# Kernel tuning notes

Measured on AMD Instinct MI355X. Metric: run time of the kernel, lower is better.

Reference implementation:

```python
import jax, jax.numpy as jnp
import numpy as np

NNZ = 131072      # number of sparse 2-tuples
M = 1048576       # number of precomputed product triples for spspmm
EMB = 128


def _mlp(x, W0, b0, W1, b1):
    # MLP(emb_dim, emb_dim, mlplayer=2, tailact=True): linear+ReLU twice
    h = jax.nn.relu(x @ W0 + b0)
    return jax.nn.relu(h @ W1 + b1)


def setup_inputs() -> dict:
    key = jax.random.key(0)
    ks = jax.random.split(key, 8)
    s = 1.0 / np.sqrt(EMB)
    Xv = jax.random.normal(ks[0], (NNZ, EMB), dtype=jnp.float32)
    W1_0 = jax.random.normal(ks[1], (EMB, EMB), dtype=jnp.float32) * s
    W1_1 = jax.random.normal(ks[2], (EMB, EMB), dtype=jnp.float32) * s
    W2_0 = jax.random.normal(ks[3], (EMB, EMB), dtype=jnp.float32) * s
    W2_1 = jax.random.normal(ks[4], (EMB, EMB), dtype=jnp.float32) * s
    b = jnp.zeros((EMB,), dtype=jnp.float32)
    ind_a = jax.random.randint(ks[5], (M,), 0, NNZ, dtype=jnp.int32)
    ind_b = jax.random.randint(ks[6], (M,), 0, NNZ, dtype=jnp.int32)
    ind_out = jax.random.randint(ks[7], (M,), 0, NNZ, dtype=jnp.int32)
    return {"Xv": Xv, "W1_0": W1_0, "b1_0": b, "W1_1": W1_1, "b1_1": b,
            "W2_0": W2_0, "b2_0": b, "W2_1": W2_1, "b2_1": b,
            "ind_a": ind_a, "ind_b": ind_b, "ind_out": ind_out}


def reference(Xv, W1_0, b1_0, W1_1, b1_1, W2_0, b2_0, W2_1, b2_1,
              ind_a, ind_b, ind_out):
    # tuplewise MLP transforms
    X1 = _mlp(Xv, W1_0, b1_0, W1_1, b1_1)   # [nnz, emb]
    X2 = _mlp(Xv, W2_0, b2_0, W2_1, b2_1)   # [nnz, emb]
    # messagepassing_tuple with sum aggregation (sparse spspmm via
    # precomputed product triples): out[t] += X1[a] * X2[b]
    prod = X1[ind_a] * X2[ind_b]            # [M, emb]
    out = jax.ops.segment_sum(prod, ind_out, num_segments=NNZ)  # [nnz, emb]
    return out
```

## Files before the change

kernel.cpp:

```cpp
#include <hip/hip_runtime.h>
#include <hip/hip_bf16.h>

#define NNZ 131072
#define MT  1048576
#define EMB 128
#define CAP 32

typedef __attribute__((ext_vector_type(8))) short  short8;
typedef __attribute__((ext_vector_type(4))) float  floatx4;

__device__ __forceinline__ ushort f2bf(float f) {
    unsigned u = __float_as_uint(f);
    u = (u + 0x7FFFu + ((u >> 16) & 1u)) >> 16;
    return (ushort)u;
}

__global__ __launch_bounds__(256) void pack_hist_kernel(
    const float* __restrict__ W10, const float* __restrict__ W11,
    const float* __restrict__ W20, const float* __restrict__ W21,
    ushort* __restrict__ Wpk,
    const int* __restrict__ io, int* __restrict__ cnt)
{
    if (blockIdx.x < 32) {
        int s = blockIdx.x * 256 + threadIdx.x;
        int L = s >> 11, sl = s & 2047;
        const float* W = (L == 0) ? W10 : (L == 1) ? W11 : (L == 2) ? W20 : W21;
        int lane = sl & 63, nk = sl >> 6;
        int col  = (nk >> 2) * 16 + (lane & 15);
        int krow = (nk & 3) * 32 + (lane >> 4) * 8;
        short8 w;
        #pragma unroll
        for (int j = 0; j < 8; ++j)
            w[j] = (short)f2bf(W[(krow + j) * EMB + col]);
        *(short8*)&Wpk[(size_t)s * 8] = w;
    } else {
        int i = (blockIdx.x - 32) * 256 + threadIdx.x;
        atomicAdd(&cnt[io[i]], 1);
    }
}

__global__ __launch_bounds__(512) void mlp_fused(
    const float* __restrict__ Xv, const ushort* __restrict__ Wpk,
    const float* __restrict__ b10, const float* __restrict__ b11,
    const float* __restrict__ b20, const float* __restrict__ b21,
    ushort* __restrict__ X1b, ushort* __restrict__ X2b,
    int do_scatter, const int* __restrict__ io, const int* __restrict__ ia,
    const int* __restrict__ ib, int* __restrict__ cur, int2* __restrict__ pairs)
{
    __shared__ ushort Wp[16384];
    __shared__ ushort Hs[16384];

    const int tid  = threadIdx.x;
    const int wave = tid >> 6;
    const int lane = tid & 63;
    const int g    = lane >> 4;
    const int r    = lane & 15;
    const int rowbase = blockIdx.x * 128 + wave * 16;
    char* hw = (char*)(Hs + wave * 2048);

    auto doScatter = [&]() {
        int base = (int)blockIdx.x * 1024 + tid;
        #pragma unroll
        for (int k = 0; k < 2; ++k) {
            int t = base + k * 512;
            int o = io[t];
            int p = atomicAdd(&cur[o], 1);
            pairs[(size_t)o * CAP + p] = make_int2(ia[t], ib[t]);
        }
    };
    const bool scatFirst = do_scatter && (blockIdx.x & 1);
    if (scatFirst) doScatter();

    short8 af[4];
    {
        const float* xsrc = Xv + (size_t)(rowbase + r) * EMB;
        #pragma unroll
        for (int kt = 0; kt < 4; ++kt) {
            const float4* p = (const float4*)(xsrc + kt * 32 + g * 8);
            float4 v0 = p[0], v1 = p[1];
            short8 a;
            a[0] = (short)f2bf(v0.x); a[1] = (short)f2bf(v0.y);
            a[2] = (short)f2bf(v0.z); a[3] = (short)f2bf(v0.w);
            a[4] = (short)f2bf(v1.x); a[5] = (short)f2bf(v1.y);
            a[6] = (short)f2bf(v1.z); a[7] = (short)f2bf(v1.w);
            af[kt] = a;
        }
    }

    auto stageW = [&](int L) {
        const ushort* src = Wpk + (size_t)L * 16384;
        #pragma unroll
        for (int s = tid; s < 2048; s += 512)
            *(short8*)&Wp[s * 8] = *(const short8*)&src[(size_t)s * 8];
    };

    floatx4 acc[8];
    auto runMFMA = [&](const short8* a4) {
        #pragma unroll
        for (int n = 0; n < 8; ++n) {
            floatx4 c = {0.f, 0.f, 0.f, 0.f};
            #pragma unroll
            for (int kt = 0; kt < 4; ++kt) {
                short8 b = *(const short8*)&Wp[((n * 4 + kt) * 64 + lane) * 8];
                c = __builtin_amdgcn_mfma_f32_16x16x32_bf16(b, a4[kt], c, 0, 0, 0);
            }
            acc[n] = c;
        }
    };

    auto epi = [&](const float* __restrict__ bias) {
        #pragma unroll
        for (int n = 0; n < 8; ++n) {
            float4 bv = *(const float4*)&bias[n * 16 + g * 4];
            ushort4 w;
            w.x = f2bf(fmaxf(acc[n][0] + bv.x, 0.f));
            w.y = f2bf(fmaxf(acc[n][1] + bv.y, 0.f));
            w.z = f2bf(fmaxf(acc[n][2] + bv.z, 0.f));
            w.w = f2bf(fmaxf(acc[n][3] + bv.w, 0.f));
            int byte = r * 256 + n * 32 + g * 8;
            byte ^= ((r & 3) << 5) ^ ((r & 4) << 2);
            *(ushort4*)(hw + byte) = w;
        }
    };

    auto loadH = [&](short8* h4) {
        #pragma unroll
        for (int kt = 0; kt < 4; ++kt) {
            int byte = r * 256 + kt * 64 + g * 16;
            byte ^= ((r & 3) << 5) ^ ((r & 4) << 2);
            h4[kt] = *(const short8*)(hw + byte);
        }
    };

    auto storeG = [&](ushort* __restrict__ dst) {
        #pragma unroll
        for (int it = 0; it < 4; ++it) {
            int row  = it * 4 + g;
            int byte = row * 256 + (lane & 15) * 16;
            byte ^= ((row & 3) << 5) ^ ((row & 4) << 2);
            short8 v = *(const short8*)(hw + byte);
            *(short8*)&dst[(size_t)rowbase * EMB + row * EMB + (lane & 15) * 8] = v;
        }
    };

    short8 h4[4];

    stageW(0); __syncthreads();
    runMFMA(af); epi(b10); __syncthreads();
    stageW(1); loadH(h4); __syncthreads();
    runMFMA(h4); epi(b11); __syncthreads();
    stageW(2); storeG(X1b); __syncthreads();
    runMFMA(af); epi(b20); __syncthreads();
    stageW(3); loadH(h4); __syncthreads();
    runMFMA(h4); epi(b21); __syncthreads();
    storeG(X2b);

    if (do_scatter && !scatFirst) doScatter();
}

__global__ __launch_bounds__(1024) void scan_kernel(
    const int* __restrict__ cnt, int* __restrict__ ptr)
{
    __shared__ int part[1024];
    int tid = threadIdx.x;
    const int4* c4 = (const int4*)(cnt + tid * 128);
    int s = 0;
    #pragma unroll 8
    for (int j = 0; j < 32; ++j) { int4 v = c4[j]; s += v.x + v.y + v.z + v.w; }
    part[tid] = s;
    __syncthreads();
    for (int off = 1; off < 1024; off <<= 1) {
        int v = (tid >= off) ? part[tid - off] : 0;
        __syncthreads();
        part[tid] += v;
        __syncthreads();
    }
    int run = part[tid] - s;
    int4* p4 = (int4*)(ptr + tid * 128);
    #pragma unroll 8
    for (int j = 0; j < 32; ++j) {
        int4 v = c4[j]; int4 w;
        w.x = run; run += v.x;
        w.y = run; run += v.y;
        w.z = run; run += v.z;
        w.w = run; run += v.w;
        p4[j] = w;
    }
    if (tid == 1023) ptr[NNZ] = run;
}

__global__ __launch_bounds__(256) void scatter_kernel(
    const int* __restrict__ io, const int* __restrict__ ia,
    const int* __restrict__ ib, const int* __restrict__ ptr,
    int* __restrict__ cur, int2* __restrict__ pairs)
{
    int t = blockIdx.x * 256 + threadIdx.x;
    int o = io[t];
    int p = atomicAdd(&cur[o], 1);
    pairs[ptr[o] + p] = make_int2(ia[t], ib[t]);
}

__global__ __launch_bounds__(256) void gather_kernel(
    const ushort* __restrict__ X1b, const ushort* __restrict__ X2b,
    const int2* __restrict__ pairs, const int* __restrict__ ptr,
    const int* __restrict__ cnt, int cap, float* __restrict__ out)
{
    int o    = blockIdx.x * 4 + (threadIdx.x >> 6);
    int lane = threadIdx.x & 63;
    int beg, end;
    if (cap) { beg = o * cap; end = beg + cnt[o]; }
    else     { beg = ptr[o];  end = ptr[o + 1]; }
    float ax = 0.f, ay = 0.f;
    for (int base = beg; base < end; base += 8) {
        #pragma unroll
        for (int e = 0; e < 8; ++e) {
            bool ok = (base + e) < end;
            int idx = ok ? base + e : beg;
            int2 p = pairs[idx];
            unsigned u1 = *(const unsigned*)(X1b + (size_t)p.x * EMB + lane * 2);
            unsigned u2 = *(const unsigned*)(X2b + (size_t)p.y * EMB + lane * 2);
            if (!ok) u1 = 0u;
            ax += __uint_as_float(u1 << 16) * __uint_as_float(u2 << 16);
            ay += __uint_as_float(u1 & 0xffff0000u) * __uint_as_float(u2 & 0xffff0000u);
        }
    }
    *(float2*)(out + (size_t)o * EMB + lane * 2) = make_float2(ax, ay);
}

extern "C" void kernel_launch(void* const* d_in, const int* in_sizes, int n_in,
                              void* d_out, int out_size, void* d_ws, size_t ws_size,
                              hipStream_t stream)
{
    (void)in_sizes; (void)n_in; (void)out_size;

    const float* Xv  = (const float*)d_in[0];
    const float* W10 = (const float*)d_in[1];
    const float* b10 = (const float*)d_in[2];
    const float* W11 = (const float*)d_in[3];
    const float* b11 = (const float*)d_in[4];
    const float* W20 = (const float*)d_in[5];
    const float* b20 = (const float*)d_in[6];
    const float* W21 = (const float*)d_in[7];
    const float* b21 = (const float*)d_in[8];
    const int*   ia  = (const int*)d_in[9];
    const int*   ib  = (const int*)d_in[10];
    const int*   io  = (const int*)d_in[11];
    float* out = (float*)d_out;

    char* ws = (char*)d_ws;
    ushort* X1b  = (ushort*)(ws);
    ushort* X2b  = (ushort*)(ws + 33554432);
    ushort* Wpk  = (ushort*)(ws + 67108864);
    int*    cur  = (int*)(ws + 67371008);
    int*    cnt  = (int*)(ws + 67895296);
    int*    ptr  = (int*)(ws + 68419584);
    int2*   pairs= (int2*)(ws + 68944000);

    const bool bucket = ws_size >= 102498432ULL;

    hipMemsetAsync(cur, 0, 524288, stream);

    if (bucket) {
        pack_hist_kernel<<<32, 256, 0, stream>>>(W10, W11, W20, W21, Wpk, io, cnt);
        mlp_fused<<<1024, 512, 0, stream>>>(Xv, Wpk, b10, b11, b20, b21,
                                            X1b, X2b, 1, io, ia, ib, cur, pairs);
        gather_kernel<<<NNZ / 4, 256, 0, stream>>>(X1b, X2b, pairs, ptr, cur,
                                                   CAP, out);
    } else {
        hipMemsetAsync(cnt, 0, 524288, stream);
        pack_hist_kernel<<<32 + MT / 256, 256, 0, stream>>>(W10, W11, W20, W21,
                                                            Wpk, io, cnt);
        mlp_fused<<<1024, 512, 0, stream>>>(Xv, Wpk, b10, b11, b20, b21,
                                            X1b, X2b, 0, io, ia, ib, cur, pairs);
        scan_kernel<<<1, 1024, 0, stream>>>(cnt, ptr);
        scatter_kernel<<<MT / 256, 256, 0, stream>>>(io, ia, ib, ptr, cur, pairs);
        gather_kernel<<<NNZ / 4, 256, 0, stream>>>(X1b, X2b, pairs, ptr, cnt,
                                                   0, out);
    }
}
```

Measured before the change: 178.0 us.

## Split bucket scatter out of MLP kernel and shrink MLP blocks for occupancy

Moves the bucket scatter (atomic slot allocation plus pair writes) out of the fused MLP kernel into its own vectorized kernel that handles four tuples per thread. The MLP kernel shrinks from 512 threads covering 128 rows to 256 threads covering 64 rows, with half the shared H buffer and a launch bound of three blocks per CU, to raise occupancy. The memset of the cursor array is folded into the weight-pack kernel, removing one API call. The cost is an extra kernel launch and losing the overlap of scatter atomics with MFMA work inside one kernel, and the weights are staged into LDS twice as many times in total.

```diff
diff --git a/kernel.cpp b/kernel.cpp
--- a/kernel.cpp
+++ b/kernel.cpp
@@ -13,6 +13,28 @@
     unsigned u = __float_as_uint(f);
     u = (u + 0x7FFFu + ((u >> 16) & 1u)) >> 16;
     return (ushort)u;
+}
+
+__global__ __launch_bounds__(256) void pack_zero_kernel(
+    const float* __restrict__ W10, const float* __restrict__ W11,
+    const float* __restrict__ W20, const float* __restrict__ W21,
+    ushort* __restrict__ Wpk, int* __restrict__ cur)
+{
+    int s = blockIdx.x * 256 + threadIdx.x;
+    int L = s >> 11, sl = s & 2047;
+    const float* W = (L == 0) ? W10 : (L == 1) ? W11 : (L == 2) ? W20 : W21;
+    int lane = sl & 63, nk = sl >> 6;
+    int col  = (nk >> 2) * 16 + (lane & 15);
+    int krow = (nk & 3) * 32 + (lane >> 4) * 8;
+    short8 w;
+    #pragma unroll
+    for (int j = 0; j < 8; ++j)
+        w[j] = (short)f2bf(W[(krow + j) * EMB + col]);
+    *(short8*)&Wpk[(size_t)s * 8] = w;
+
+    int4* dst = (int4*)(cur) + s * 4;
+    int4 z = make_int4(0, 0, 0, 0);
+    dst[0] = z; dst[1] = z; dst[2] = z; dst[3] = z;
 }
 
 __global__ __launch_bounds__(256) void pack_hist_kernel(
@@ -39,37 +61,41 @@
     }
 }
 
-__global__ __launch_bounds__(512) void mlp_fused(
+__global__ __launch_bounds__(256) void scatter_bucket(
+    const int* __restrict__ io, const int* __restrict__ ia,
+    const int* __restrict__ ib, int* __restrict__ cur,
+    int2* __restrict__ pairs)
+{
+    int i = blockIdx.x * 256 + threadIdx.x;
+    int4 o4 = ((const int4*)io)[i];
+    int4 a4 = ((const int4*)ia)[i];
+    int4 b4 = ((const int4*)ib)[i];
+    int p0 = atomicAdd(&cur[o4.x], 1);
+    int p1 = atomicAdd(&cur[o4.y], 1);
+    int p2 = atomicAdd(&cur[o4.z], 1);
+    int p3 = atomicAdd(&cur[o4.w], 1);
+    pairs[(size_t)o4.x * CAP + p0] = make_int2(a4.x, b4.x);
+    pairs[(size_t)o4.y * CAP + p1] = make_int2(a4.y, b4.y);
+    pairs[(size_t)o4.z * CAP + p2] = make_int2(a4.z, b4.z);
+    pairs[(size_t)o4.w * CAP + p3] = make_int2(a4.w, b4.w);
+}
+
+__global__ __launch_bounds__(256, 3) void mlp_kernel(
     const float* __restrict__ Xv, const ushort* __restrict__ Wpk,
     const float* __restrict__ b10, const float* __restrict__ b11,
     const float* __restrict__ b20, const float* __restrict__ b21,
-    ushort* __restrict__ X1b, ushort* __restrict__ X2b,
-    int do_scatter, const int* __restrict__ io, const int* __restrict__ ia,
-    const int* __restrict__ ib, int* __restrict__ cur, int2* __restrict__ pairs)
+    ushort* __restrict__ X1b, ushort* __restrict__ X2b)
 {
     __shared__ ushort Wp[16384];
-    __shared__ ushort Hs[16384];
+    __shared__ ushort Hs[8192];
 
     const int tid  = threadIdx.x;
     const int wave = tid >> 6;
     const int lane = tid & 63;
     const int g    = lane >> 4;
     const int r    = lane & 15;
-    const int rowbase = blockIdx.x * 128 + wave * 16;
+    const int rowbase = blockIdx.x * 64 + wave * 16;
     char* hw = (char*)(Hs + wave * 2048);
-
-    auto doScatter = [&]() {
-        int base = (int)blockIdx.x * 1024 + tid;
-        #pragma unroll
-        for (int k = 0; k < 2; ++k) {
-            int t = base + k * 512;
-            int o = io[t];
-            int p = atomicAdd(&cur[o], 1);
-            pairs[(size_t)o * CAP + p] = make_int2(ia[t], ib[t]);
-        }
-    };
-    const bool scatFirst = do_scatter && (blockIdx.x & 1);
-    if (scatFirst) doScatter();
 
     short8 af[4];
     {
@@ -90,7 +116,7 @@
     auto stageW = [&](int L) {
         const ushort* src = Wpk + (size_t)L * 16384;
         #pragma unroll
-        for (int s = tid; s < 2048; s += 512)
+        for (int s = tid; s < 2048; s += 256)
             *(short8*)&Wp[s * 8] = *(const short8*)&src[(size_t)s * 8];
     };
 
@@ -154,8 +180,6 @@
     stageW(3); loadH(h4); __syncthreads();
     runMFMA(h4); epi(b21); __syncthreads();
     storeG(X2b);
-
-    if (do_scatter && !scatFirst) doScatter();
 }
 
 __global__ __launch_bounds__(1024) void scan_kernel(
@@ -189,7 +213,7 @@
     if (tid == 1023) ptr[NNZ] = run;
 }
 
-__global__ __launch_bounds__(256) void scatter_kernel(
+__global__ __launch_bounds__(256) void scatter_csr(
     const int* __restrict__ io, const int* __restrict__ ia,
     const int* __restrict__ ib, const int* __restrict__ ptr,
     int* __restrict__ cur, int2* __restrict__ pairs)
@@ -258,22 +282,22 @@
 
     const bool bucket = ws_size >= 102498432ULL;
 
-    hipMemsetAsync(cur, 0, 524288, stream);
-
     if (bucket) {
-        pack_hist_kernel<<<32, 256, 0, stream>>>(W10, W11, W20, W21, Wpk, io, cnt);
-        mlp_fused<<<1024, 512, 0, stream>>>(Xv, Wpk, b10, b11, b20, b21,
-                                            X1b, X2b, 1, io, ia, ib, cur, pairs);
+        pack_zero_kernel<<<32, 256, 0, stream>>>(W10, W11, W20, W21, Wpk, cur);
+        scatter_bucket<<<1024, 256, 0, stream>>>(io, ia, ib, cur, pairs);
+        mlp_kernel<<<2048, 256, 0, stream>>>(Xv, Wpk, b10, b11, b20, b21,
+                                             X1b, X2b);
         gather_kernel<<<NNZ / 4, 256, 0, stream>>>(X1b, X2b, pairs, ptr, cur,
                                                    CAP, out);
     } else {
+        hipMemsetAsync(cur, 0, 524288, stream);
         hipMemsetAsync(cnt, 0, 524288, stream);
         pack_hist_kernel<<<32 + MT / 256, 256, 0, stream>>>(W10, W11, W20, W21,
                                                             Wpk, io, cnt);
-        mlp_fused<<<1024, 512, 0, stream>>>(Xv, Wpk, b10, b11, b20, b21,
-                                            X1b, X2b, 0, io, ia, ib, cur, pairs);
+        mlp_kernel<<<2048, 256, 0, stream>>>(Xv, Wpk, b10, b11, b20, b21,
+                                             X1b, X2b);
         scan_kernel<<<1, 1024, 0, stream>>>(cnt, ptr);
-        scatter_kernel<<<MT / 256, 256, 0, stream>>>(io, ia, ib, ptr, cur, pairs);
+        scatter_csr<<<MT / 256, 256, 0, stream>>>(io, ia, ib, ptr, cur, pairs);
         gather_kernel<<<NNZ / 4, 256, 0, stream>>>(X1b, X2b, pairs, ptr, cnt,
                                                    0, out);
     }
```

New measurement: 215.2 us. 1.21x slower.
